# Optimization experiments

Hardware: AMD Instinct MI355X
Metric: run time of the kernel (lower is better)

## Reference

```python
import jax, jax.numpy as jnp
import numpy as np

N, E, T, Q, G = 50000, 800000, 1000000, 1000000, 4096
L, H, D, HID, ED = 3, 8, 16, 128, 16
EPS = 1e-8


def setup_inputs() -> dict:
    key = jax.random.key(0)
    ks = jax.random.split(key, 20)
    inp = {
        "x": jax.random.normal(ks[0], (N, HID), jnp.float32),
        "pos": jax.random.normal(ks[1], (N, 3), jnp.float32),
        "edge_attr": jax.random.normal(ks[2], (E, ED), jnp.float32),
        "temps": jax.random.uniform(ks[3], (G, 1), jnp.float32),
        "edge_index": jax.random.randint(ks[4], (2, E), 0, N, jnp.int32),
        "triple_index": jax.random.randint(ks[5], (3, T), 0, N, jnp.int32),
        "quadra_index": jax.random.randint(ks[6], (4, Q), 0, N, jnp.int32),
        "batch": jnp.sort(jax.random.randint(ks[7], (N,), 0, G, jnp.int32)),
        "W": jax.random.normal(ks[8], (L, HID, HID), jnp.float32) * 0.08,
        "a_e": jax.random.normal(ks[9], (L, H, 2 * D + 1), jnp.float32) * 0.1,
        "a_t": jax.random.normal(ks[10], (L, H, 2 * D + 1), jnp.float32) * 0.1,
        "a_q": jax.random.normal(ks[11], (L, H, 2 * D + 1), jnp.float32) * 0.1,
        "We": jax.random.normal(ks[12], (L, ED, H), jnp.float32) * 0.1,
        "W1": jax.random.normal(ks[13], (2 * HID + 1, 256), jnp.float32) * 0.06,
        "b1": jnp.zeros((256,), jnp.float32),
        "W2": jax.random.normal(ks[14], (256, 256), jnp.float32) * 0.06,
        "b2": jnp.zeros((256,), jnp.float32),
        "W3": jax.random.normal(ks[15], (256, 1), jnp.float32) * 0.06,
        "b3": jnp.zeros((1,), jnp.float32),
    }
    return inp


def _seg_softmax(logits, seg, n):
    # numerically stable segment softmax over destination nodes
    m = jax.ops.segment_max(logits, seg, num_segments=n)
    m = jnp.where(jnp.isfinite(m), m, 0.0)
    e = jnp.exp(logits - m[seg])
    s = jax.ops.segment_sum(e, seg, num_segments=n)
    return e / (s[seg] + 1e-16)


def _hop(hh, src, dst, geom, a, bias=None):
    # hh: [N,H,D]; gather-attend-scatter for one interaction order
    q, k = hh[dst], hh[src]                      # [M,H,D]
    logits = jnp.einsum('mhd,hd->mh', q, a[:, :D]) \
           + jnp.einsum('mhd,hd->mh', k, a[:, D:2 * D]) \
           + geom[:, None] * a[:, 2 * D]
    if bias is not None:
        logits = logits + bias
    logits = jax.nn.leaky_relu(logits, 0.2)
    alpha = _seg_softmax(logits, dst, hh.shape[0])  # [M,H]
    return jax.ops.segment_sum(k * alpha[..., None], dst, num_segments=hh.shape[0])


def _geom_features(pos, edge_index, triple_index, quadra_index):
    # edge distance
    d = jnp.linalg.norm(pos[edge_index[0]] - pos[edge_index[1]] + EPS, axis=-1)
    # triple angle cos at center node j of (i,j,k)
    i, j, k = triple_index
    u, v = pos[i] - pos[j], pos[k] - pos[j]
    cos_a = (u * v).sum(-1) / (jnp.linalg.norm(u, axis=-1) * jnp.linalg.norm(v, axis=-1) + EPS)
    # quadra dihedral cos of (p0,p1,p2,p3)
    p0, p1, p2, p3 = pos[quadra_index[0]], pos[quadra_index[1]], pos[quadra_index[2]], pos[quadra_index[3]]
    b1, b2, b3 = p1 - p0, p2 - p1, p3 - p2
    n1, n2 = jnp.cross(b1, b2), jnp.cross(b2, b3)
    cos_d = (n1 * n2).sum(-1) / (jnp.linalg.norm(n1, axis=-1) * jnp.linalg.norm(n2, axis=-1) + EPS)
    return d, cos_a, cos_d


def reference(x, pos, edge_attr, temps, edge_index, triple_index, quadra_index, batch,
              W, a_e, a_t, a_q, We, W1, b1, W2, b2, W3, b3):
    d, cos_a, cos_d = _geom_features(pos, edge_index, triple_index, quadra_index)
    e_src, e_dst = edge_index[1], edge_index[0]
    t_src, t_dst = triple_index[2], triple_index[0]
    q_src, q_dst = quadra_index[3], quadra_index[0]
    h = x
    for l in range(L):
        hl = h @ W[l]                              # [N,HID]
        hh = hl.reshape(N, H, D)
        bias_e = edge_attr @ We[l]                 # [E,H]
        agg = _hop(hh, e_src, e_dst, d, a_e[l], bias_e) \
            + _hop(hh, t_src, t_dst, cos_a, a_t[l]) \
            + _hop(hh, q_src, q_dst, cos_d, a_q[l])
        h = jax.nn.elu(hl + agg.reshape(N, HID))
    # readout: sum + max pooling per graph, concat temperature scalar
    s = jax.ops.segment_sum(h, batch, num_segments=G)
    mx = jax.ops.segment_max(h, batch, num_segments=G)
    mx = jnp.where(jnp.isfinite(mx), mx, 0.0)
    mol = jnp.concatenate([s, mx, temps], axis=-1)  # [G, 2*HID+1]
    hdn = jax.nn.elu(mol @ W1 + b1)
    hdn = jax.nn.elu(hdn @ W2 + b2)
    return hdn @ W3 + b3
```

## Files before the change

### kernel.cpp

```cpp
#include <hip/hip_runtime.h>
#include <hip/hip_fp16.h>

#define NN 50000
#define EE 800000
#define TT 1000000
#define QQ 1000000
#define GG 4096
#define HID 128
#define NH 8
#define DH 16
#define CAP 64
#define SLOT 5

#define TILE 2048
#define KPT 8
#define NB 196
#define NBG 392

typedef unsigned int u32;
typedef unsigned int u32x4 __attribute__((ext_vector_type(4)));

__device__ __forceinline__ float eluf(float x){ return x > 0.f ? x : expm1f(x); }

__device__ __forceinline__ u32 pack_sg(int src, float g){
  return ((u32)src << 16) | (u32)__half_as_ushort(__float2half(g));
}
__device__ __forceinline__ float lo16(u32 w){ return __half2float(__ushort_as_half((unsigned short)(w&0xFFFFu))); }
__device__ __forceinline__ float hi16(u32 w){ return __half2float(__ushort_as_half((unsigned short)(w>>16))); }
__device__ __forceinline__ u32 packf2(float a, float b){
  __half2 h = __floats2half2_rn(a,b);
  return *(u32*)&h;
}
__device__ __forceinline__ void unpack8(const __half* p, float* o){
  u32x4 w = *(const u32x4*)p;
  #pragma unroll
  for (int j=0;j<4;j++){ u32 x=w[j]; o[2*j]=lo16(x); o[2*j+1]=hi16(x); }
}

__global__ void k_count3(const int* __restrict__ ei, const int* __restrict__ ti, const int* __restrict__ qi,
                         int* __restrict__ cnt){
  int i = blockIdx.x*blockDim.x + threadIdx.x;
  if (i < EE) atomicAdd(&cnt[ei[i]], 1);
  else if (i < EE+TT) atomicAdd(&cnt[NN + ti[i-EE]], 1);
  else if (i < EE+TT+QQ) atomicAdd(&cnt[2*NN + qi[i-EE-TT]], 1);
}

__global__ __launch_bounds__(1024) void k_scan4(const int* __restrict__ cnt,
    int* __restrict__ off_e, int* __restrict__ off_t, int* __restrict__ off_q,
    int* __restrict__ cur_e, int* __restrict__ cur_t, int* __restrict__ cur_q,
    const int* __restrict__ batch, int* __restrict__ goff){
  int b = blockIdx.x, t = threadIdx.x;
  if (b == 3){
    for (int g=t; g<=GG; g+=1024){
      int lo=0, hi=NN;
      while (lo<hi){ int mid=(lo+hi)>>1; if (batch[mid]<g) lo=mid+1; else hi=mid; }
      goff[g]=lo;
    }
    return;
  }
  __shared__ int part[1024];
  const int* c = cnt + b*NN;
  int* off = (b==0)?off_e:(b==1)?off_t:off_q;
  int* cur = (b==0)?cur_e:(b==1)?cur_t:cur_q;
  int chunk = (NN + 1023) >> 10;
  int s0 = t*chunk, s1 = min(NN, s0+chunk);
  int sum = 0;
  for (int i=s0;i<s1;i++) sum += c[i];
  part[t] = sum;
  __syncthreads();
  for (int d=1; d<1024; d<<=1){
    int v = (t>=d) ? part[t-d] : 0;
    __syncthreads();
    part[t] += v;
    __syncthreads();
  }
  int run = (t==0) ? 0 : part[t-1];
  for (int i=s0;i<s1;i++){ off[i]=run; cur[i]=run; run += c[i]; }
  if (t==0) off[NN] = part[1023];
}

__global__ void k_fillE(const float* __restrict__ pos, const float* __restrict__ edge_attr,
    const int* __restrict__ ei, const float* __restrict__ We,
    int* __restrict__ cur_e, u32* __restrict__ eRec){
  int i = blockIdx.x*blockDim.x + threadIdx.x;
  if (i >= EE) return;
  int dn = ei[i], sn = ei[EE+i];
  float dx = pos[dn*3+0]-pos[sn*3+0]+1e-8f;
  float dy = pos[dn*3+1]-pos[sn*3+1]+1e-8f;
  float dz = pos[dn*3+2]-pos[sn*3+2]+1e-8f;
  float d = sqrtf(dx*dx+dy*dy+dz*dz);
  int p = atomicAdd(&cur_e[dn], 1);
  const float4* s = (const float4*)(edge_attr + (size_t)i*16);
  float4 v0=s[0], v1=s[1], v2=s[2], v3=s[3];
  float a[16] = {v0.x,v0.y,v0.z,v0.w, v1.x,v1.y,v1.z,v1.w,
                 v2.x,v2.y,v2.z,v2.w, v3.x,v3.y,v3.z,v3.w};
  u32x4 r[4];
  r[0][0] = pack_sg(sn, d); r[0][1]=0; r[0][2]=0; r[0][3]=0;
  #pragma unroll
  for (int l=0; l<3; l++){
    const float* Wel = We + l*DH*NH;
    #pragma unroll
    for (int hp=0; hp<4; hp++){
      float sa=0.f, sb=0.f;
      #pragma unroll
      for (int c=0;c<16;c++){
        sa = fmaf(a[c], Wel[c*NH + 2*hp],     sa);
        sb = fmaf(a[c], Wel[c*NH + 2*hp + 1], sb);
      }
      r[1+l][hp] = packf2(sa, sb);
    }
  }
  u32x4* dst4 = (u32x4*)(eRec + (size_t)p*16);
  dst4[0]=r[0]; dst4[1]=r[1]; dst4[2]=r[2]; dst4[3]=r[3];
}

__global__ __launch_bounds__(256) void k_fillTQ_A(const float* __restrict__ pos,
    const int* __restrict__ ti, const int* __restrict__ qi,
    const int* __restrict__ off_t, const int* __restrict__ off_q,
    u32* __restrict__ gcur, uint2* __restrict__ stg){
  __shared__ u32 s_sg[TILE];
  __shared__ u32 s_dw[TILE];
  __shared__ u32 s_cnt[NBG];
  __shared__ u32 s_scan[512];
  __shared__ u32 s_gb[NBG];
  int t = threadIdx.x;
  size_t tile0 = (size_t)blockIdx.x * TILE;
  for (int i=t;i<NBG;i+=256) s_cnt[i]=0;
  __syncthreads();
  u32 my_sg[KPT], my_dw[KPT], my_rank[KPT]; int my_bg[KPT];
  #pragma unroll
  for (int k=0;k<KPT;k++){
    size_t idx = tile0 + (size_t)k*256 + t;
    my_bg[k] = -1;
    if (idx < (size_t)TT+QQ){
      int dst, src; float g;
      int typeq = (idx >= (size_t)TT);
      if (!typeq){
        int m = (int)idx;
        int ia=ti[m], jb=ti[TT+m], kc=ti[2*TT+m];
        float ux=pos[ia*3+0]-pos[jb*3+0], uy=pos[ia*3+1]-pos[jb*3+1], uz=pos[ia*3+2]-pos[jb*3+2];
        float vx=pos[kc*3+0]-pos[jb*3+0], vy=pos[kc*3+1]-pos[jb*3+1], vz=pos[kc*3+2]-pos[jb*3+2];
        float num = ux*vx+uy*vy+uz*vz;
        float den = sqrtf(ux*ux+uy*uy+uz*uz)*sqrtf(vx*vx+vy*vy+vz*vz) + 1e-8f;
        g = num/den; dst = ia; src = kc;
      } else {
        int m = (int)(idx - TT);
        int p0=qi[m], p1=qi[QQ+m], p2=qi[2*QQ+m], p3=qi[3*QQ+m];
        float b1x=pos[p1*3+0]-pos[p0*3+0], b1y=pos[p1*3+1]-pos[p0*3+1], b1z=pos[p1*3+2]-pos[p0*3+2];
        float b2x=pos[p2*3+0]-pos[p1*3+0], b2y=pos[p2*3+1]-pos[p1*3+1], b2z=pos[p2*3+2]-pos[p1*3+2];
        float b3x=pos[p3*3+0]-pos[p2*3+0], b3y=pos[p3*3+1]-pos[p2*3+1], b3z=pos[p3*3+2]-pos[p2*3+2];
        float n1x=b1y*b2z-b1z*b2y, n1y=b1z*b2x-b1x*b2z, n1z=b1x*b2y-b1y*b2x;
        float n2x=b2y*b3z-b2z*b3y, n2y=b2z*b3x-b2x*b3z, n2z=b2x*b3y-b2y*b3x;
        float num = n1x*n2x+n1y*n2y+n1z*n2z;
        float den = sqrtf(n1x*n1x+n1y*n1y+n1z*n1z)*sqrtf(n2x*n2x+n2y*n2y+n2z*n2z) + 1e-8f;
        g = num/den; dst = p0; src = p3;
      }
      int bg = (typeq?NB:0) + (dst>>8);
      my_sg[k] = pack_sg(src, g);
      my_dw[k] = (u32)dst | ((u32)typeq<<20);
      my_bg[k] = bg;
      my_rank[k] = atomicAdd(&s_cnt[bg], 1u);
    }
  }
  __syncthreads();
  int i0=t, i1=t+256;
  s_scan[i0] = (i0<NBG)? s_cnt[i0] : 0u;
  s_scan[i1] = (i1<NBG)? s_cnt[i1] : 0u;
  __syncthreads();
  for (int d=1; d<512; d<<=1){
    u32 a0 = (i0>=d)? s_scan[i0-d] : 0u;
    u32 a1 = (i1>=d)? s_scan[i1-d] : 0u;
    __syncthreads();
    s_scan[i0]+=a0; s_scan[i1]+=a1;
    __syncthreads();
  }
  u32 total = s_scan[NBG-1];
  #pragma unroll
  for (int k=0;k<KPT;k++){
    if (my_bg[k]>=0){
      u32 slot = s_scan[my_bg[k]] - s_cnt[my_bg[k]] + my_rank[k];
      s_sg[slot]=my_sg[k]; s_dw[slot]=my_dw[k];
    }
  }
  for (int i=t;i<NBG;i+=256)
    s_gb[i] = s_cnt[i] ? atomicAdd(&gcur[i], s_cnt[i]) : 0u;
  __syncthreads();
  for (u32 j=t; j<total; j+=256){
    u32 dw = s_dw[j];
    int typeq = (dw>>20)&1;
    int dst = dw & 0xFFFFF;
    int bg = (typeq?NB:0) + (dst>>8);
    u32 rank = j - (s_scan[bg]-s_cnt[bg]);
    int w0 = (typeq? bg-NB : bg)*256;
    size_t sbase = typeq ? (size_t)TT + (size_t)off_q[w0] : (size_t)off_t[w0];
    stg[sbase + s_gb[bg] + rank] = make_uint2(s_sg[j], dw);
  }
}

__global__ __launch_bounds__(256) void k_fillTQ_B(const uint2* __restrict__ stg,
    const int* __restrict__ off_t, const int* __restrict__ off_q,
    u32* __restrict__ csg_t, u32* __restrict__ csg_q){
  __shared__ int curL[256];
  int b = blockIdx.x, t = threadIdx.x;
  int typeq = (b>=NB);
  int bl = typeq? b-NB : b;
  const int* off = typeq? off_q : off_t;
  u32* csg = typeq? csg_q : csg_t;
  int w0 = bl*256, w1 = min(w0+256, NN);
  int s0 = off[w0], s1 = off[w1];
  for (int i=t; i<w1-w0; i+=256) curL[i] = off[w0+i];
  __syncthreads();
  size_t sb = (typeq? (size_t)TT : 0) + (size_t)s0;
  int cnt = s1 - s0;
  for (int i=t; i<cnt; i+=256){
    uint2 r = stg[sb+i];
    int dst = r.y & 0xFFFFF;
    int p = atomicAdd(&curL[dst-w0], 1);
    csg[p] = r.x;
  }
}

#define GR 16
__global__ __launch_bounds__(128) void k_gemm(const float* __restrict__ A, const float* __restrict__ Wm,
    const float* __restrict__ ae, const float* __restrict__ at, const float* __restrict__ aq,
    __half* __restrict__ B16,
    __half* __restrict__ qa_e, __half* __restrict__ ka_e,
    __half* __restrict__ qa_t, __half* __restrict__ ka_t,
    __half* __restrict__ qa_q, __half* __restrict__ ka_q){
  __shared__ float sh[GR][132];
  int col = threadIdx.x;
  int r0 = blockIdx.x * GR;
  const float* Ab = A + (size_t)r0*HID;
  float acc[GR];
  #pragma unroll
  for (int r=0;r<GR;r++) acc[r]=0.f;
  #pragma unroll 4
  for (int k=0;k<HID;k++){
    float wv = Wm[k*HID+col];
    #pragma unroll
    for (int r=0;r<GR;r++) acc[r] = fmaf(Ab[r*HID+k], wv, acc[r]);
  }
  #pragma unroll
  for (int r=0;r<GR;r++){
    B16[(size_t)(r0+r)*HID+col] = __float2half(acc[r]);
    sh[r][col] = acc[r];
  }
  __syncthreads();
  int r = threadIdx.x>>3, h = threadIdx.x&7;
  float x[DH];
  #pragma unroll
  for (int j=0;j<DH;j++) x[j] = sh[r][h*DH+j];
  const float* Ae = ae + h*33; const float* At_ = at + h*33; const float* Aq = aq + h*33;
  float s0=0,s1=0,s2=0,s3=0,s4=0,s5=0;
  #pragma unroll
  for (int d=0; d<DH; d++){
    s0 = fmaf(x[d], Ae[d],      s0);  s1 = fmaf(x[d], Ae[DH+d],  s1);
    s2 = fmaf(x[d], At_[d],     s2);  s3 = fmaf(x[d], At_[DH+d], s3);
    s4 = fmaf(x[d], Aq[d],      s4);  s5 = fmaf(x[d], Aq[DH+d],  s5);
  }
  size_t o = (size_t)(r0+r)*NH + h;
  qa_e[o]=__float2half(s0); ka_e[o]=__float2half(s1);
  qa_t[o]=__float2half(s2); ka_t[o]=__float2half(s3);
  qa_q[o]=__float2half(s4); ka_q[o]=__float2half(s5);
}

__global__ __launch_bounds__(256) void k_hop3(
    const int* __restrict__ off_e, const int* __restrict__ off_t, const int* __restrict__ off_q,
    const u32* __restrict__ eRec,
    const u32* __restrict__ csg_t, const u32* __restrict__ csg_q,
    const __half* __restrict__ qa_e, const __half* __restrict__ ka_e,
    const __half* __restrict__ qa_t, const __half* __restrict__ ka_t,
    const __half* __restrict__ qa_q, const __half* __restrict__ ka_q,
    const float* __restrict__ ae, const float* __restrict__ at, const float* __restrict__ aq,
    const __half* __restrict__ hh16, const __half* __restrict__ hlr16, float* __restrict__ hout,
    int L, int nwaves){
  __shared__ u32 sw[4][3*CAP*SLOT];
  int t = threadIdx.x;
  int wv = t>>6, l = t&63;
  u32* Wb = sw[wv];
  int lg = l>>4, ld = l&15;
  int wiR = ld>>2;
  int shR = ((ld>>1)&1)*16;
  float cfE[8], cfT[8], cfQ[8];
  #pragma unroll
  for (int h=0;h<8;h++){ cfE[h]=ae[h*33+32]; cfT[h]=at[h*33+32]; cfQ[h]=aq[h*33+32]; }
  for (int n = blockIdx.x*4 + wv; n < NN; n += nwaves){
    int se=off_e[n], de=off_e[n+1]-se;
    int st=off_t[n], dt=off_t[n+1]-st;
    int sq=off_q[n], dq=off_q[n+1]-sq;
    float accE[8]={0,0,0,0,0,0,0,0}, accT[8]={0,0,0,0,0,0,0,0}, accQ[8]={0,0,0,0,0,0,0,0};
    float dE=0.f, dT=0.f, dQ=0.f;
    int maxd = max(de, max(dt, dq));
    for (int base=0; base<maxd; base+=CAP){
      int ce = min(CAP, de-base); if (ce<0) ce=0;
      int ct = min(CAP, dt-base); if (ct<0) ct=0;
      int cq = min(CAP, dq-base); if (cq<0) cq=0;
      if (l < ce){
        size_t idx = (size_t)(se+base+l);
        u32 sg = eRec[idx*16];
        u32x4 br = *(const u32x4*)(eRec + idx*16 + 4 + 4*L);
        int src = (int)(sg>>16);
        float g = lo16(sg);
        float ka8[8]; unpack8(ka_e + (size_t)src*NH, ka8);
        float qa8[8]; unpack8(qa_e + (size_t)n*NH, qa8);
        u32* sl = Wb + l*SLOT;
        #pragma unroll
        for (int j=0;j<4;j++){
          u32 bw = br[j];
          float l0 = qa8[2*j]   + ka8[2*j]   + g*cfE[2*j]   + lo16(bw);
          float l1 = qa8[2*j+1] + ka8[2*j+1] + g*cfE[2*j+1] + hi16(bw);
          l0 = l0>=0.f ? l0 : 0.2f*l0;
          l1 = l1>=0.f ? l1 : 0.2f*l1;
          sl[j] = packf2(__expf(l0), __expf(l1));
        }
        sl[4] = (u32)src;
      }
      if (l < ct){
        u32 sg = csg_t[(size_t)(st+base+l)];
        int src = (int)(sg>>16);
        float g = lo16(sg);
        float ka8[8]; unpack8(ka_t + (size_t)src*NH, ka8);
        float qa8[8]; unpack8(qa_t + (size_t)n*NH, qa8);
        u32* sl = Wb + CAP*SLOT + l*SLOT;
        #pragma unroll
        for (int j=0;j<4;j++){
          float l0 = qa8[2*j]   + ka8[2*j]   + g*cfT[2*j];
          float l1 = qa8[2*j+1] + ka8[2*j+1] + g*cfT[2*j+1];
          l0 = l0>=0.f ? l0 : 0.2f*l0;
          l1 = l1>=0.f ? l1 : 0.2f*l1;
          sl[j] = packf2(__expf(l0), __expf(l1));
        }
        sl[4] = (u32)src;
      }
      if (l < cq){
        u32 sg = csg_q[(size_t)(sq+base+l)];
        int src = (int)(sg>>16);
        float g = lo16(sg);
        float ka8[8]; unpack8(ka_q + (size_t)src*NH, ka8);
        float qa8[8]; unpack8(qa_q + (size_t)n*NH, qa8);
        u32* sl = Wb + 2*CAP*SLOT + l*SLOT;
        #pragma unroll
        for (int j=0;j<4;j++){
          float l0 = qa8[2*j]   + ka8[2*j]   + g*cfQ[2*j];
          float l1 = qa8[2*j+1] + ka8[2*j+1] + g*cfQ[2*j+1];
          l0 = l0>=0.f ? l0 : 0.2f*l0;
          l1 = l1>=0.f ? l1 : 0.2f*l1;
          sl[j] = packf2(__expf(l0), __expf(l1));
        }
        sl[4] = (u32)src;
      }
      __builtin_amdgcn_wave_barrier();
      {
        int maxc = max(ce, max(ct, cq));
        #pragma unroll 2
        for (int m=0;m<maxc;m+=4){
          int r = m+lg;
          if (r < ce){
            const u32* P = Wb;
            u32 aw = P[r*SLOT+wiR];
            u32 sr = P[r*SLOT+4];
            float am = __half2float(__ushort_as_half((unsigned short)(aw>>shR)));
            u32x4 v = *(const u32x4*)(hh16 + (size_t)sr*HID + ld*8);
            dE += am;
            #pragma unroll
            for (int j=0;j<4;j++){
              u32 w = v[j];
              accE[2*j]   = fmaf(lo16(w), am, accE[2*j]);
              accE[2*j+1] = fmaf(hi16(w), am, accE[2*j+1]);
            }
          }
          if (r < ct){
            const u32* P = Wb + CAP*SLOT;
            u32 aw = P[r*SLOT+wiR];
            u32 sr = P[r*SLOT+4];
            float am = __half2float(__ushort_as_half((unsigned short)(aw>>shR)));
            u32x4 v = *(const u32x4*)(hh16 + (size_t)sr*HID + ld*8);
            dT += am;
            #pragma unroll
            for (int j=0;j<4;j++){
              u32 w = v[j];
              accT[2*j]   = fmaf(lo16(w), am, accT[2*j]);
              accT[2*j+1] = fmaf(hi16(w), am, accT[2*j+1]);
            }
          }
          if (r < cq){
            const u32* P = Wb + 2*CAP*SLOT;
            u32 aw = P[r*SLOT+wiR];
            u32 sr = P[r*SLOT+4];
            float am = __half2float(__ushort_as_half((unsigned short)(aw>>shR)));
            u32x4 v = *(const u32x4*)(hh16 + (size_t)sr*HID + ld*8);
            dQ += am;
            #pragma unroll
            for (int j=0;j<4;j++){
              u32 w = v[j];
              accQ[2*j]   = fmaf(lo16(w), am, accQ[2*j]);
              accQ[2*j+1] = fmaf(hi16(w), am, accQ[2*j+1]);
            }
          }
        }
      }
      __builtin_amdgcn_wave_barrier();
    }
    #pragma unroll
    for (int j=0;j<8;j++){
      accE[j] += __shfl_xor(accE[j],16); accE[j] += __shfl_xor(accE[j],32);
      accT[j] += __shfl_xor(accT[j],16); accT[j] += __shfl_xor(accT[j],32);
      accQ[j] += __shfl_xor(accQ[j],16); accQ[j] += __shfl_xor(accQ[j],32);
    }
    dE += __shfl_xor(dE,16); dE += __shfl_xor(dE,32);
    dT += __shfl_xor(dT,16); dT += __shfl_xor(dT,32);
    dQ += __shfl_xor(dQ,16); dQ += __shfl_xor(dQ,32);
    if (lg == 0){
      float invE = 1.f/(dE + 1e-16f);
      float invT = 1.f/(dT + 1e-16f);
      float invQ = 1.f/(dQ + 1e-16f);
      float ov[8];
      #pragma unroll
      for (int j=0;j<8;j++) ov[j] = accE[j]*invE + accT[j]*invT + accQ[j]*invQ;
      size_t oi = (size_t)n*HID + ld*8;
      u32x4 rv = *(const u32x4*)(hlr16 + oi);
      float r8[8];
      #pragma unroll
      for (int j=0;j<4;j++){ u32 w=rv[j]; r8[2*j]=lo16(w); r8[2*j+1]=hi16(w); }
      float4 w0 = make_float4(eluf(r8[0]+ov[0]), eluf(r8[1]+ov[1]), eluf(r8[2]+ov[2]), eluf(r8[3]+ov[3]));
      float4 w1 = make_float4(eluf(r8[4]+ov[4]), eluf(r8[5]+ov[5]), eluf(r8[6]+ov[6]), eluf(r8[7]+ov[7]));
      *(float4*)(hout+oi)   = w0;
      *(float4*)(hout+oi+4) = w1;
    }
  }
}

__global__ __launch_bounds__(128) void k_pool(const float* __restrict__ h, const int* __restrict__ goff,
                                              float* __restrict__ gs, float* __restrict__ gmx){
  int g = blockIdx.x, t = threadIdx.x;
  int s = goff[g], e = goff[g+1];
  float sum = 0.f, mx = -INFINITY;
  for (int n=s; n<e; n++){
    float v = h[(size_t)n*HID+t];
    sum += v; mx = fmaxf(mx, v);
  }
  gs[(size_t)g*HID+t] = sum;
  gmx[(size_t)g*HID+t] = (s < e) ? mx : 0.f;
}

#define GPB 8
#define MSTR 260
__global__ __launch_bounds__(256) void k_mlp(const float* __restrict__ gs, const float* __restrict__ gmx,
    const float* __restrict__ temps,
    const float* __restrict__ W1, const float* __restrict__ b1,
    const float* __restrict__ W2, const float* __restrict__ b2,
    const float* __restrict__ W3, const float* __restrict__ b3,
    float* __restrict__ out){
  __shared__ float mol[GPB][MSTR];
  __shared__ float hd[GPB][MSTR];
  int g0 = blockIdx.x*GPB, t = threadIdx.x;
  for (int i=t; i<GPB*HID; i+=256){
    int g=i>>7, d=i&127;
    mol[g][d]     = gs[(size_t)(g0+g)*HID+d];
    mol[g][128+d] = gmx[(size_t)(g0+g)*HID+d];
  }
  if (t < GPB){ mol[t][256]=temps[g0+t]; mol[t][257]=0.f; mol[t][258]=0.f; mol[t][259]=0.f; }
  __syncthreads();
  float acc[GPB];
  #pragma unroll
  for (int g=0;g<GPB;g++) acc[g]=b1[t];
  for (int k0=0;k0<256;k0+=4){
    float w0=W1[(size_t)(k0+0)*256+t], w1=W1[(size_t)(k0+1)*256+t];
    float w2=W1[(size_t)(k0+2)*256+t], w3=W1[(size_t)(k0+3)*256+t];
    #pragma unroll
    for (int g=0;g<GPB;g++){
      float4 m4 = *(const float4*)&mol[g][k0];
      acc[g] = fmaf(m4.x,w0, fmaf(m4.y,w1, fmaf(m4.z,w2, fmaf(m4.w,w3, acc[g]))));
    }
  }
  { float wl=W1[(size_t)256*256+t];
    #pragma unroll
    for (int g=0;g<GPB;g++) acc[g]=fmaf(mol[g][256],wl,acc[g]); }
  #pragma unroll
  for (int g=0;g<GPB;g++) hd[g][t]=eluf(acc[g]);
  __syncthreads();
  #pragma unroll
  for (int g=0;g<GPB;g++) acc[g]=b2[t];
  for (int k0=0;k0<256;k0+=4){
    float w0=W2[(size_t)(k0+0)*256+t], w1=W2[(size_t)(k0+1)*256+t];
    float w2=W2[(size_t)(k0+2)*256+t], w3=W2[(size_t)(k0+3)*256+t];
    #pragma unroll
    for (int g=0;g<GPB;g++){
      float4 h4 = *(const float4*)&hd[g][k0];
      acc[g] = fmaf(h4.x,w0, fmaf(h4.y,w1, fmaf(h4.z,w2, fmaf(h4.w,w3, acc[g]))));
    }
  }
  float w3v = W3[t];
  #pragma unroll
  for (int g=0;g<GPB;g++) mol[g][t] = eluf(acc[g])*w3v;
  __syncthreads();
  int g = t >> 5, j = t & 31;
  float s = 0.f;
  for (int i=j; i<256; i+=32) s += mol[g][i];
  #pragma unroll
  for (int d=16; d>0; d>>=1) s += __shfl_down(s, d, 32);
  if (j == 0) out[g0+g] = s + b3[0];
}

extern "C" void kernel_launch(void* const* d_in, const int* in_sizes, int n_in,
                              void* d_out, int out_size, void* d_ws, size_t ws_size,
                              hipStream_t stream){
  const float* x         = (const float*)d_in[0];
  const float* pos       = (const float*)d_in[1];
  const float* edge_attr = (const float*)d_in[2];
  const float* temps     = (const float*)d_in[3];
  const int*   ei        = (const int*)d_in[4];
  const int*   ti        = (const int*)d_in[5];
  const int*   qi        = (const int*)d_in[6];
  const int*   batch     = (const int*)d_in[7];
  const float* W         = (const float*)d_in[8];
  const float* a_e       = (const float*)d_in[9];
  const float* a_t       = (const float*)d_in[10];
  const float* a_q       = (const float*)d_in[11];
  const float* We        = (const float*)d_in[12];
  const float* W1        = (const float*)d_in[13];
  const float* b1        = (const float*)d_in[14];
  const float* W2        = (const float*)d_in[15];
  const float* b2        = (const float*)d_in[16];
  const float* W3        = (const float*)d_in[17];
  const float* b3        = (const float*)d_in[18];
  float* out = (float*)d_out;

  char* base = (char*)d_ws; size_t woff = 0;
  auto alloc = [&](size_t bytes)->void*{
    void* p = base + woff;
    woff = (woff + bytes + 255) & ~(size_t)255;
    return p;
  };
  float*  hbuf   = (float*)alloc((size_t)NN*HID*4);
  __half* hl16   = (__half*)alloc((size_t)NN*HID*2);
  __half* qa_e   = (__half*)alloc((size_t)NN*NH*2);
  __half* ka_e   = (__half*)alloc((size_t)NN*NH*2);
  __half* qa_t   = (__half*)alloc((size_t)NN*NH*2);
  __half* ka_t   = (__half*)alloc((size_t)NN*NH*2);
  __half* qa_q   = (__half*)alloc((size_t)NN*NH*2);
  __half* ka_q   = (__half*)alloc((size_t)NN*NH*2);
  u32*    eRec   = (u32*)alloc((size_t)EE*64);
  u32*    csg_t  = (u32*)alloc((size_t)TT*4);
  u32*    csg_q  = (u32*)alloc((size_t)QQ*4);
  uint2*  stg    = (uint2*)alloc((size_t)(TT+QQ)*8);
  float*  gs     = (float*)alloc((size_t)GG*HID*4);
  float*  gmx    = (float*)alloc((size_t)GG*HID*4);
  int*    cnt    = (int*)alloc((size_t)3*NN*4);
  u32*    gcur   = (u32*)alloc((size_t)NBG*4);
  int*    off_e  = (int*)alloc((size_t)(NN+1)*4);
  int*    off_t  = (int*)alloc((size_t)(NN+1)*4);
  int*    off_q  = (int*)alloc((size_t)(NN+1)*4);
  int*    cur_e  = (int*)alloc((size_t)NN*4);
  int*    cur_t  = (int*)alloc((size_t)NN*4);
  int*    cur_q  = (int*)alloc((size_t)NN*4);
  int*    goff   = (int*)alloc((size_t)(GG+1)*4);

  hipMemsetAsync(cnt, 0, (size_t)3*NN*4, stream);
  hipMemsetAsync(gcur, 0, (size_t)NBG*4, stream);
  int tot = EE+TT+QQ;
  k_count3<<<(tot+255)/256,256,0,stream>>>(ei, ti, qi, cnt);
  k_scan4<<<4,1024,0,stream>>>(cnt, off_e, off_t, off_q, cur_e, cur_t, cur_q, batch, goff);
  k_fillE<<<(EE+255)/256,256,0,stream>>>(pos, edge_attr, ei, We, cur_e, eRec);
  k_fillTQ_A<<<(TT+QQ+TILE-1)/TILE,256,0,stream>>>(pos, ti, qi, off_t, off_q, gcur, stg);
  k_fillTQ_B<<<NBG,256,0,stream>>>(stg, off_t, off_q, csg_t, csg_q);

  int hopBlocks = 2048;
  int nwaves = hopBlocks*4;
  for (int l=0; l<3; l++){
    const float* hin = (l==0) ? x : hbuf;
    k_gemm<<<NN/GR,128,0,stream>>>(hin, W + (size_t)l*HID*HID,
                                   a_e+l*264, a_t+l*264, a_q+l*264,
                                   hl16, qa_e, ka_e, qa_t, ka_t, qa_q, ka_q);
    k_hop3<<<hopBlocks,256,0,stream>>>(off_e, off_t, off_q, eRec, csg_t, csg_q,
                                       qa_e, ka_e, qa_t, ka_t, qa_q, ka_q,
                                       a_e+l*264, a_t+l*264, a_q+l*264,
                                       hl16, hl16, hbuf, l, nwaves);
  }

  k_pool<<<GG,128,0,stream>>>(hbuf, goff, gs, gmx);
  k_mlp<<<GG/GPB,256,0,stream>>>(gs, gmx, temps, W1, b1, W2, b2, W3, b3, out);
}
```

Baseline: 1.046 ms.

## Concatenate three hops into one window and pre-normalize attention weights

The hop kernel now lays out edge, triple and quad neighbours of a node in one contiguous window of up to 192 entries instead of three separate 64-entry buffers. Softmax denominators are computed in a first pass over shared memory, and the weights are scaled by the inverse before aggregation. This leaves one accumulator set instead of three, cutting register pressure and lanes idled when the hop degrees differ. The cost is a serial denominator loop on 24 lanes and, for nodes with more than 192 neighbours, recomputing the logits.

```diff
diff --git a/kernel.cpp b/kernel.cpp
--- a/kernel.cpp
+++ b/kernel.cpp
@@ -9,8 +9,8 @@
 #define HID 128
 #define NH 8
 #define DH 16
-#define CAP 64
 #define SLOT 5
+#define WCAP 192
 
 #define TILE 2048
 #define KPT 8
@@ -274,128 +274,127 @@
     const float* __restrict__ ae, const float* __restrict__ at, const float* __restrict__ aq,
     const __half* __restrict__ hh16, const __half* __restrict__ hlr16, float* __restrict__ hout,
     int L, int nwaves){
-  __shared__ u32 sw[4][3*CAP*SLOT];
+  __shared__ u32 sw[4][WCAP*SLOT + 32];
   int t = threadIdx.x;
   int wv = t>>6, l = t&63;
   u32* Wb = sw[wv];
+  float* invB = (float*)(Wb + WCAP*SLOT);
   int lg = l>>4, ld = l&15;
   int wiR = ld>>2;
   int shR = ((ld>>1)&1)*16;
+  int headR = ld>>1;
+  int dh_hop = l>>3, dh_head = l&7;
   float cfE[8], cfT[8], cfQ[8];
   #pragma unroll
   for (int h=0;h<8;h++){ cfE[h]=ae[h*33+32]; cfT[h]=at[h*33+32]; cfQ[h]=aq[h*33+32]; }
+
   for (int n = blockIdx.x*4 + wv; n < NN; n += nwaves){
     int se=off_e[n], de=off_e[n+1]-se;
     int st=off_t[n], dt=off_t[n+1]-st;
     int sq=off_q[n], dq=off_q[n+1]-sq;
-    float accE[8]={0,0,0,0,0,0,0,0}, accT[8]={0,0,0,0,0,0,0,0}, accQ[8]={0,0,0,0,0,0,0,0};
-    float dE=0.f, dT=0.f, dQ=0.f;
-    int maxd = max(de, max(dt, dq));
-    for (int base=0; base<maxd; base+=CAP){
-      int ce = min(CAP, de-base); if (ce<0) ce=0;
-      int ct = min(CAP, dt-base); if (ct<0) ct=0;
-      int cq = min(CAP, dq-base); if (cq<0) cq=0;
-      if (l < ce){
-        size_t idx = (size_t)(se+base+l);
-        u32 sg = eRec[idx*16];
-        u32x4 br = *(const u32x4*)(eRec + idx*16 + 4 + 4*L);
-        int src = (int)(sg>>16);
-        float g = lo16(sg);
-        float ka8[8]; unpack8(ka_e + (size_t)src*NH, ka8);
-        float qa8[8]; unpack8(qa_e + (size_t)n*NH, qa8);
-        u32* sl = Wb + l*SLOT;
-        #pragma unroll
-        for (int j=0;j<4;j++){
-          u32 bw = br[j];
-          float l0 = qa8[2*j]   + ka8[2*j]   + g*cfE[2*j]   + lo16(bw);
-          float l1 = qa8[2*j+1] + ka8[2*j+1] + g*cfE[2*j+1] + hi16(bw);
-          l0 = l0>=0.f ? l0 : 0.2f*l0;
-          l1 = l1>=0.f ? l1 : 0.2f*l1;
-          sl[j] = packf2(__expf(l0), __expf(l1));
+    int b1 = de, b2 = de+dt, D = b2+dq;
+    bool fits = (D <= WCAP);
+
+    auto LOGITS = [&](int win, int wc){
+      for (int sub=0; sub<wc; sub+=64){
+        int s = sub + l;
+        if (s < wc){
+          int c = win + s;
+          u32* sl = Wb + s*SLOT;
+          if (c < b1){
+            size_t idx = (size_t)(se + c);
+            u32 sg = eRec[idx*16];
+            u32x4 br = *(const u32x4*)(eRec + idx*16 + 4 + 4*L);
+            int src = (int)(sg>>16);
+            float g = lo16(sg);
+            float ka8[8]; unpack8(ka_e + (size_t)src*NH, ka8);
+            float qa8[8]; unpack8(qa_e + (size_t)n*NH, qa8);
+            #pragma unroll
+            for (int j=0;j<4;j++){
+              u32 bw = br[j];
+              float l0 = qa8[2*j]   + ka8[2*j]   + g*cfE[2*j]   + lo16(bw);
+              float l1 = qa8[2*j+1] + ka8[2*j+1] + g*cfE[2*j+1] + hi16(bw);
+              l0 = l0>=0.f ? l0 : 0.2f*l0;
+              l1 = l1>=0.f ? l1 : 0.2f*l1;
+              sl[j] = packf2(__expf(l0), __expf(l1));
+            }
+            sl[4] = (u32)src;
+          } else if (c < b2){
+            u32 sg = csg_t[(size_t)(st + (c-b1))];
+            int src = (int)(sg>>16);
+            float g = lo16(sg);
+            float ka8[8]; unpack8(ka_t + (size_t)src*NH, ka8);
+            float qa8[8]; unpack8(qa_t + (size_t)n*NH, qa8);
+            #pragma unroll
+            for (int j=0;j<4;j++){
+              float l0 = qa8[2*j]   + ka8[2*j]   + g*cfT[2*j];
+              float l1 = qa8[2*j+1] + ka8[2*j+1] + g*cfT[2*j+1];
+              l0 = l0>=0.f ? l0 : 0.2f*l0;
+              l1 = l1>=0.f ? l1 : 0.2f*l1;
+              sl[j] = packf2(__expf(l0), __expf(l1));
+            }
+            sl[4] = (u32)src;
+          } else {
+            u32 sg = csg_q[(size_t)(sq + (c-b2))];
+            int src = (int)(sg>>16);
+            float g = lo16(sg);
+            float ka8[8]; unpack8(ka_q + (size_t)src*NH, ka8);
+            float qa8[8]; unpack8(qa_q + (size_t)n*NH, qa8);
+            #pragma unroll
+            for (int j=0;j<4;j++){
+              float l0 = qa8[2*j]   + ka8[2*j]   + g*cfQ[2*j];
+              float l1 = qa8[2*j+1] + ka8[2*j+1] + g*cfQ[2*j+1];
+              l0 = l0>=0.f ? l0 : 0.2f*l0;
+              l1 = l1>=0.f ? l1 : 0.2f*l1;
+              sl[j] = packf2(__expf(l0), __expf(l1));
+            }
+            sl[4] = (u32)src;
+          }
         }
-        sl[4] = (u32)src;
       }
-      if (l < ct){
-        u32 sg = csg_t[(size_t)(st+base+l)];
-        int src = (int)(sg>>16);
-        float g = lo16(sg);
-        float ka8[8]; unpack8(ka_t + (size_t)src*NH, ka8);
-        float qa8[8]; unpack8(qa_t + (size_t)n*NH, qa8);
-        u32* sl = Wb + CAP*SLOT + l*SLOT;
-        #pragma unroll
-        for (int j=0;j<4;j++){
-          float l0 = qa8[2*j]   + ka8[2*j]   + g*cfT[2*j];
-          float l1 = qa8[2*j+1] + ka8[2*j+1] + g*cfT[2*j+1];
-          l0 = l0>=0.f ? l0 : 0.2f*l0;
-          l1 = l1>=0.f ? l1 : 0.2f*l1;
-          sl[j] = packf2(__expf(l0), __expf(l1));
+    };
+
+    float dsum = 0.f;
+    int dh_lo = (dh_hop==0)?0:(dh_hop==1)?b1:b2;
+    int dh_hi = (dh_hop==0)?b1:(dh_hop==1)?b2:D;
+    for (int win=0; win<D; win+=WCAP){
+      int wc = min(WCAP, D-win);
+      LOGITS(win, wc);
+      __builtin_amdgcn_wave_barrier();
+      if (l < 24){
+        int rlo = max(dh_lo, win) - win;
+        int rhi = min(dh_hi, win+wc) - win;
+        int wsel = dh_head>>1, hsel = (dh_head&1)*16;
+        for (int r=rlo; r<rhi; r++){
+          u32 w = Wb[r*SLOT + wsel];
+          dsum += __half2float(__ushort_as_half((unsigned short)(w>>hsel)));
         }
-        sl[4] = (u32)src;
-      }
-      if (l < cq){
-        u32 sg = csg_q[(size_t)(sq+base+l)];
-        int src = (int)(sg>>16);
-        float g = lo16(sg);
-        float ka8[8]; unpack8(ka_q + (size_t)src*NH, ka8);
-        float qa8[8]; unpack8(qa_q + (size_t)n*NH, qa8);
-        u32* sl = Wb + 2*CAP*SLOT + l*SLOT;
-        #pragma unroll
-        for (int j=0;j<4;j++){
-          float l0 = qa8[2*j]   + ka8[2*j]   + g*cfQ[2*j];
-          float l1 = qa8[2*j+1] + ka8[2*j+1] + g*cfQ[2*j+1];
-          l0 = l0>=0.f ? l0 : 0.2f*l0;
-          l1 = l1>=0.f ? l1 : 0.2f*l1;
-          sl[j] = packf2(__expf(l0), __expf(l1));
-        }
-        sl[4] = (u32)src;
       }
       __builtin_amdgcn_wave_barrier();
-      {
-        int maxc = max(ce, max(ct, cq));
-        #pragma unroll 2
-        for (int m=0;m<maxc;m+=4){
-          int r = m+lg;
-          if (r < ce){
-            const u32* P = Wb;
-            u32 aw = P[r*SLOT+wiR];
-            u32 sr = P[r*SLOT+4];
-            float am = __half2float(__ushort_as_half((unsigned short)(aw>>shR)));
-            u32x4 v = *(const u32x4*)(hh16 + (size_t)sr*HID + ld*8);
-            dE += am;
-            #pragma unroll
-            for (int j=0;j<4;j++){
-              u32 w = v[j];
-              accE[2*j]   = fmaf(lo16(w), am, accE[2*j]);
-              accE[2*j+1] = fmaf(hi16(w), am, accE[2*j+1]);
-            }
-          }
-          if (r < ct){
-            const u32* P = Wb + CAP*SLOT;
-            u32 aw = P[r*SLOT+wiR];
-            u32 sr = P[r*SLOT+4];
-            float am = __half2float(__ushort_as_half((unsigned short)(aw>>shR)));
-            u32x4 v = *(const u32x4*)(hh16 + (size_t)sr*HID + ld*8);
-            dT += am;
-            #pragma unroll
-            for (int j=0;j<4;j++){
-              u32 w = v[j];
-              accT[2*j]   = fmaf(lo16(w), am, accT[2*j]);
-              accT[2*j+1] = fmaf(hi16(w), am, accT[2*j+1]);
-            }
-          }
-          if (r < cq){
-            const u32* P = Wb + 2*CAP*SLOT;
-            u32 aw = P[r*SLOT+wiR];
-            u32 sr = P[r*SLOT+4];
-            float am = __half2float(__ushort_as_half((unsigned short)(aw>>shR)));
-            u32x4 v = *(const u32x4*)(hh16 + (size_t)sr*HID + ld*8);
-            dQ += am;
-            #pragma unroll
-            for (int j=0;j<4;j++){
-              u32 w = v[j];
-              accQ[2*j]   = fmaf(lo16(w), am, accQ[2*j]);
-              accQ[2*j+1] = fmaf(hi16(w), am, accQ[2*j+1]);
-            }
+    }
+    if (l < 24) invB[l] = 1.f/(dsum + 1e-16f);
+    __builtin_amdgcn_wave_barrier();
+
+    float acc[8] = {0,0,0,0,0,0,0,0};
+    for (int win=0; win<D; win+=WCAP){
+      int wc = min(WCAP, D-win);
+      if (!fits){ LOGITS(win, wc); __builtin_amdgcn_wave_barrier(); }
+      #pragma unroll 2
+      for (int m=0; m<wc; m+=4){
+        int r = m+lg;
+        if (r < wc){
+          int c = win + r;
+          int hop = (c<b1)?0:(c<b2)?1:2;
+          u32 aw = Wb[r*SLOT+wiR];
+          u32 sr = Wb[r*SLOT+4];
+          float am = __half2float(__ushort_as_half((unsigned short)(aw>>shR)))
+                   * invB[hop*8 + headR];
+          u32x4 v = *(const u32x4*)(hh16 + (size_t)sr*HID + ld*8);
+          #pragma unroll
+          for (int j=0;j<4;j++){
+            u32 w = v[j];
+            acc[2*j]   = fmaf(lo16(w), am, acc[2*j]);
+            acc[2*j+1] = fmaf(hi16(w), am, acc[2*j+1]);
           }
         }
       }
@@ -403,27 +402,17 @@
     }
     #pragma unroll
     for (int j=0;j<8;j++){
-      accE[j] += __shfl_xor(accE[j],16); accE[j] += __shfl_xor(accE[j],32);
-      accT[j] += __shfl_xor(accT[j],16); accT[j] += __shfl_xor(accT[j],32);
-      accQ[j] += __shfl_xor(accQ[j],16); accQ[j] += __shfl_xor(accQ[j],32);
-    }
-    dE += __shfl_xor(dE,16); dE += __shfl_xor(dE,32);
-    dT += __shfl_xor(dT,16); dT += __shfl_xor(dT,32);
-    dQ += __shfl_xor(dQ,16); dQ += __shfl_xor(dQ,32);
+      acc[j] += __shfl_xor(acc[j],16);
+      acc[j] += __shfl_xor(acc[j],32);
+    }
     if (lg == 0){
-      float invE = 1.f/(dE + 1e-16f);
-      float invT = 1.f/(dT + 1e-16f);
-      float invQ = 1.f/(dQ + 1e-16f);
-      float ov[8];
-      #pragma unroll
-      for (int j=0;j<8;j++) ov[j] = accE[j]*invE + accT[j]*invT + accQ[j]*invQ;
       size_t oi = (size_t)n*HID + ld*8;
       u32x4 rv = *(const u32x4*)(hlr16 + oi);
       float r8[8];
       #pragma unroll
       for (int j=0;j<4;j++){ u32 w=rv[j]; r8[2*j]=lo16(w); r8[2*j+1]=hi16(w); }
-      float4 w0 = make_float4(eluf(r8[0]+ov[0]), eluf(r8[1]+ov[1]), eluf(r8[2]+ov[2]), eluf(r8[3]+ov[3]));
-      float4 w1 = make_float4(eluf(r8[4]+ov[4]), eluf(r8[5]+ov[5]), eluf(r8[6]+ov[6]), eluf(r8[7]+ov[7]));
+      float4 w0 = make_float4(eluf(r8[0]+acc[0]), eluf(r8[1]+acc[1]), eluf(r8[2]+acc[2]), eluf(r8[3]+acc[3]));
+      float4 w1 = make_float4(eluf(r8[4]+acc[4]), eluf(r8[5]+acc[5]), eluf(r8[6]+acc[6]), eluf(r8[7]+acc[7]));
       *(float4*)(hout+oi)   = w0;
       *(float4*)(hout+oi+4) = w1;
     }
```

Measured after the change: 1.072 ms. +2.4%, slower.
